# Kernel tuning notes

Hardware: AMD Instinct MI355X
Metric: run time of the kernel (lower is better)

Reference implementation:

```python
import jax, jax.numpy as jnp
import numpy as np

FS = 32000
HOP = 512
WIN_SIZES = [2048, 1024, 512, 256, 128, 64]
BAND_EDGES = [20.0, 80.0, 500.0, 1250.0, 2540.0, 4050.0, 15000.0]
ERB_STEP = 0.25
ERBS = np.arange(1.75, 39.0 + 1e-6, ERB_STEP)            # 150 ERB channels
FC = (10.0 ** (ERBS / 21.366) - 1.0) / 0.004368           # channel center freqs (Hz)
I0 = (2e-5) ** 2                                          # reference intensity (Pa^2)
LUT_X = np.linspace(0.0, 110.0, 88).astype(np.float32)    # LUT excitation grid (dB)
SIGMA = 0.08
P_INHIB = 1.5978
HALF = 8
_g = np.arange(-HALF, HALF + 1) * ERB_STEP
GAUSS = np.exp(-_g ** 2 / (2.0 * SIGMA ** 2))
GAUSS = (GAUSS / GAUSS.sum()).astype(np.float32)

def _components():
    # frequency-dependent window selection: longest window -> lowest band
    freqs, idxs = [], []
    for w, N in enumerate(WIN_SIZES):
        fb = np.arange(N // 2 + 1) * FS / N
        sel = np.where((fb >= BAND_EDGES[w]) & (fb < BAND_EDGES[w + 1]))[0]
        idxs.append(sel)
        freqs.append(fb[sel])
    return np.concatenate(freqs), idxs
COMP_FREQS, WIN_BIN_IDX = _components()  # K ~ 67 sparse components

def _roex():
    erbw = 24.673 * (0.004368 * FC + 1.0)
    p = 4.0 * FC / erbw
    g = np.abs(COMP_FREQS[:, None] / FC[None, :] - 1.0)
    return ((1.0 + p * g) * np.exp(-p * g)).astype(np.float32)
ROEX_W = _roex()  # (K, 150)

def _ear_filter(x, h):
    # Stage 1: outer/middle ear FIR, same-length output
    B, C, T = x.shape
    k = h[::-1].reshape(1, 1, -1)
    y = jax.lax.conv_general_dilated(x.reshape(B * C, 1, T), k, (1,),
                                     [(h.shape[0] // 2, h.shape[0] // 2)],
                                     dimension_numbers=("NCH", "OIH", "NCH"))
    return y.reshape(B, C, T)

def _sparse_spectrum(x):
    # Stage 2: multi-resolution FFT analysis -> linear intensities at sparse comps
    B, T = x.shape
    F = T // HOP
    pad = WIN_SIZES[0] // 2
    xp = jnp.pad(x, ((0, 0), (pad, pad)))
    centers = pad + jnp.arange(F) * HOP
    outs = []
    for N, bins in zip(WIN_SIZES, WIN_BIN_IDX):
        idx = (centers - N // 2)[:, None] + jnp.arange(N)   # (F, N)
        frames = xp[:, idx]                                 # (B, F, N)
        n = jnp.arange(N, dtype=x.dtype)
        win = 0.5 - 0.5 * jnp.cos(2.0 * jnp.pi * n / (N - 1))
        spec = jnp.fft.rfft(frames * win, axis=-1)
        amp = 2.0 * jnp.abs(spec[..., jnp.asarray(bins)]) / win.sum()
        outs.append(0.5 * amp ** 2)                          # tone intensity
    return jnp.concatenate(outs, axis=-1)                    # (B, F, K)

def _agc(x, a_att, a_rel):
    # asymmetric attack/release AGC over frame axis (axis=1)
    def step(s, xt):
        a = jnp.where(xt > s, a_att, a_rel)
        s = a * xt + (1.0 - a) * s
        return s, s
    xt = jnp.moveaxis(x, 1, 0)
    _, y = jax.lax.scan(step, jnp.zeros_like(xt[0]), xt)
    return jnp.moveaxis(y, 0, 1)

def _smooth(n):
    # Gaussian spatial smoothing along ERB-channel axis
    B, F, C = n.shape
    k = jnp.asarray(GAUSS[::-1].copy(), n.dtype).reshape(1, 1, -1)
    y = jax.lax.conv_general_dilated(n.reshape(B * F, 1, C), k, (1,),
                                     [(HALF, HALF)],
                                     dimension_numbers=("NCH", "OIH", "NCH"))
    return y.reshape(B, F, C)

def _forward(audio, ear_fir, lut_values):
    y = _ear_filter(audio, ear_fir)
    lut_x = jnp.asarray(LUT_X)
    W = jnp.asarray(ROEX_W, audio.dtype)
    stl = []
    for ch in range(2):
        I = _sparse_spectrum(y[:, ch])                       # (B, F, K)
        E = I @ W                                            # roex excitation (B, F, 150)
        E_db = 10.0 * jnp.log10(E / I0 + 1e-12)
        n_inst = jnp.interp(jnp.clip(E_db, lut_x[0], lut_x[-1]), lut_x, lut_values)
        stl.append(_agc(n_inst, 0.045, 0.033))               # short-term loudness
    sl, sr = _smooth(stl[0]), _smooth(stl[1])
    sech = lambda z: 1.0 / jnp.cosh(z)
    stl_l = (sl * sech(P_INHIB * sr)).sum(-1) / 4.0          # (B, F)
    stl_r = (sr * sech(P_INHIB * sl)).sum(-1) / 4.0
    ltl_l = _agc(stl_l[..., None], 0.01, 0.00133)[..., 0]
    ltl_r = _agc(stl_r[..., None], 0.01, 0.00133)[..., 0]
    sLoud = stl_l + stl_r
    lLoud = ltl_l + ltl_r
    mLoud = lLoud.max(axis=-1)
    return sLoud, lLoud, mLoud

def setup_inputs():
    key = jax.random.key(0)
    k1, k2, k3 = jax.random.split(key, 3)
    audio = jax.random.normal(k1, (16, 2, 320000), dtype=jnp.float32) * 0.05
    ear_fir = jax.random.normal(k2, (1025,), dtype=jnp.float32) * 0.03
    lut_values = jnp.sort(jax.random.uniform(k3, (88,), dtype=jnp.float32)) * 40.0
    return {"audio": audio, "ear_fir": ear_fir, "lut_values": lut_values}

def reference(audio, ear_fir, lut_values):
    return _forward(audio, ear_fir, lut_values)
```

## Files before the change

### kernel.cpp

```cpp
#include <hip/hip_runtime.h>
#include <hip/hip_bf16.h>
#include <math.h>

#define T_LEN   320000
#define NB      16
#define NROWS   32
#define NFRAMES 625
#define NCOMP   67
#define NCH     150
#define HOPSZ   512
#define BREP    8
#define BSZ     491520

typedef __attribute__((ext_vector_type(8))) _Float16 half8v;
typedef __attribute__((ext_vector_type(8))) short short8v;
typedef __attribute__((ext_vector_type(4))) float f32x4;

__constant__ int cW_N[6]  = {2048,1024,512,256,128,64};
__constant__ int cW_K0[6] = {2,3,8,10,11,9};
__constant__ int cW_CB[7] = {0,4,17,29,40,46,67};
__constant__ int cW_CO[7] = {0,8192,21504,27648,30464,31232,32576};
__constant__ int dNEp[6]  = {3072,2048,1536,1280,1152,1152};
__constant__ int dNEr[6]  = {3072,2048,1536,1280,1152,1088};
__constant__ int dBTb[7]  = {0,147456,245760,319488,380928,436224,491520};
__constant__ int dCPB[6]  = {12,8,6,5,5,5};
__constant__ int dCKB[7]  = {0,48,152,224,279,309,414};
__constant__ int eW[8] = {0,0,0,1,2,3,4,5};
__constant__ int eF[8] = {0,1,624,0,0,0,0,0};

__constant__ int tBb[12]   = {147456,180224,0,380928,0,436224,245760,454656,270336,473088,319488,339968};
__constant__ int tNEp[12]  = {2048,2048,3072,1152,3072,1152,1536,1152,1536,1152,1280,1280};
__constant__ int tStb[12]  = {512,512,0,960,0,992,768,992,768,992,896,896};
__constant__ int tKs0[12]  = {0,0,0,0,48,0,0,0,0,0,0,0};
__constant__ int tKs1[12]  = {64,64,48,36,96,36,48,36,48,36,40,40};
__constant__ int tJadd[12] = {4,12,0,40,0,46,17,54,25,62,29,37};
__constant__ int tNbL[12]  = {13,5,4,6,4,21,12,13,4,5,11,3};
__constant__ int tMode[12] = {0,0,1,0,2,0,0,0,0,0,0,0};
__constant__ int wStart[8] = {0,1,2,4,6,8,10,11};
__constant__ int wCnt[8]   = {1,1,2,2,2,2,1,1};

__device__ __forceinline__ unsigned short f2bf(float v) {
  unsigned u = __float_as_uint(v);
  return (unsigned short)((u + 0x7FFFu + ((u >> 16) & 1u)) >> 16);
}

__global__ __launch_bounds__(256) void setup_k(const float* __restrict__ h,
                                               const float* __restrict__ x,
                                               float2* __restrict__ coeff,
                                               float* __restrict__ Wmat,
                                               float* __restrict__ gauss,
                                               unsigned short* __restrict__ Bf,
                                               float* __restrict__ ye,
                                               unsigned short* __restrict__ Wb16) {
  __shared__ __align__(16) float sm[3585];
  const int bid = blockIdx.x, tid = threadIdx.x;
  if (bid < 167) {
    int gid = bid * 256 + tid;
    if (gid < 32576) {
      int w = 0;
      while (gid >= cW_CO[w + 1]) ++w;
      int local = gid - cW_CO[w];
      int N = cW_N[w];
      int jloc = local / N;
      int n = local - jloc * N;
      int k = cW_K0[w] + jloc;
      float win = 0.5f - 0.5f * cospif(2.0f * (float)n / (float)(N - 1));
      int r = (int)(((long long)k * (long long)n) % (long long)N);
      float ang = 2.0f * (float)r / (float)N;
      float scale = sqrtf(2.0f) / (0.5f * (float)(N - 1));
      float wc = win * scale;
      coeff[gid] = make_float2(wc * cospif(ang), wc * sinpif(ang));
    } else if (gid < 32576 + NCOMP * NCH) {
      int t = gid - 32576;
      int j = t / NCH, c = t - j * NCH;
      float erb = 1.75f + 0.25f * (float)c;
      float fc = (exp10f(erb * (1.0f / 21.366f)) - 1.0f) * (1.0f / 0.004368f);
      float erbw = 24.673f * (0.004368f * fc + 1.0f);
      float p = 4.0f * fc / erbw;
      int w = 0;
      while (j >= cW_CB[w + 1]) ++w;
      float freq = (float)(cW_K0[w] + (j - cW_CB[w])) * (32000.0f / (float)cW_N[w]);
      float g = fabsf(freq / fc - 1.0f);
      float pg = p * g;
      Wmat[j * NCH + c] = (1.0f + pg) * expf(-pg);
    } else if (gid == 32576 + NCOMP * NCH) {
      float tmp[17]; float s = 0.0f;
      for (int k = 0; k < 17; ++k) {
        float g = ((float)k - 8.0f) * 0.25f;
        tmp[k] = expf(-g * g / (2.0f * 0.08f * 0.08f));
        s += tmp[k];
      }
      for (int k = 0; k < 17; ++k) gauss[k] = tmp[k] / s;
    }
  } else if (bid < 581) {
    float* cre_l = sm;
    float* cim_l = sm + 1280;
    float* hs    = sm + 2560;
    const int b2 = bid - 167;
    int w = 0;
    while (b2 >= dCKB[w + 1]) ++w;
    const int local = b2 - dCKB[w];
    const int jloc = local / dCPB[w];
    const int chunk = local - jloc * dCPB[w];
    const int N = cW_N[w];
    const int k = cW_K0[w] + jloc;
    const int NEp = dNEp[w], NEr = dNEr[w];
    const int v0 = chunk * 256;
    const int nlo_blk = max(0, v0 - 1024);
    const int nhi_blk = min(N - 1, v0 + 255);
    const int cnt_n = nhi_blk - nlo_blk + 1;
    const float scale = sqrtf(2.0f) / (0.5f * (float)(N - 1));
    for (int i = tid; i < 1025; i += 256) hs[i] = h[i];
    for (int i = tid; i < cnt_n; i += 256) {
      int n = nlo_blk + i;
      float win = 0.5f - 0.5f * cospif(2.0f * (float)n / (float)(N - 1));
      int r = (int)(((long long)k * (long long)n) % (long long)N);
      float ang = 2.0f * (float)r / (float)N;
      float wc = win * scale;
      cre_l[i] = wc * cospif(ang);
      cim_l[i] = wc * sinpif(ang);
    }
    __syncthreads();
    const int v = v0 + tid;
    if (v >= NEp) return;
    float re = 0.0f, im = 0.0f;
    if (v < NEr) {
      const int n0 = max(nlo_blk, v - 1024);
      const int n1 = min(nhi_blk, v);
      float r0 = 0.f, r1 = 0.f, r2 = 0.f, r3 = 0.f;
      float m0 = 0.f, m1 = 0.f, m2 = 0.f, m3 = 0.f;
      int n = n0;
      const int hoff = 1024 - v, coff = -nlo_blk;
      for (; n + 3 <= n1; n += 4) {
        float h0 = hs[n + hoff],     h1 = hs[n + 1 + hoff];
        float h2 = hs[n + 2 + hoff], h3 = hs[n + 3 + hoff];
        r0 = fmaf(cre_l[n + coff],     h0, r0); m0 = fmaf(cim_l[n + coff],     h0, m0);
        r1 = fmaf(cre_l[n + 1 + coff], h1, r1); m1 = fmaf(cim_l[n + 1 + coff], h1, m1);
        r2 = fmaf(cre_l[n + 2 + coff], h2, r2); m2 = fmaf(cim_l[n + 2 + coff], h2, m2);
        r3 = fmaf(cre_l[n + 3 + coff], h3, r3); m3 = fmaf(cim_l[n + 3 + coff], h3, m3);
      }
      for (; n <= n1; ++n) {
        float hv = hs[n + hoff];
        r0 = fmaf(cre_l[n + coff], hv, r0);
        m0 = fmaf(cim_l[n + coff], hv, m0);
      }
      re = (r0 + r1) + (r2 + r3);
      im = (m0 + m1) + (m2 + m3);
    }
    size_t o0 = (size_t)dBTb[w] + (size_t)(2 * jloc) * NEp + v;
    size_t o1 = o0 + NEp;
    _Float16 hr = (_Float16)re;
    _Float16 hi2 = (_Float16)im;
    unsigned short hrb = *(unsigned short*)&hr;
    unsigned short hib = *(unsigned short*)&hi2;
#pragma unroll
    for (int cp = 0; cp < BREP; ++cp) {
      Bf[(size_t)cp * BSZ + o0] = hrb;
      Bf[(size_t)cp * BSZ + o1] = hib;
    }
  } else if (bid < 965) {
    float* xl = sm;
    float* hs = sm + 1280;
    const int b2 = bid - 581;
    const int chunk = b2 % 12, row = b2 / 12;
    const size_t rowoff = (size_t)row * T_LEN;
    const int i0 = chunk * 256;
    const int pos0 = (i0 < 1536) ? i0 : 318464 + (i0 - 1536);
    for (int i = tid; i < 1025; i += 256) hs[i] = h[i];
    for (int i = tid; i < 1280; i += 256) {
      int g = pos0 - 512 + i;
      xl[i] = ((unsigned)g < (unsigned)T_LEN) ? x[rowoff + g] : 0.0f;
    }
    __syncthreads();
    float a0 = 0.0f, a1 = 0.0f, a2 = 0.0f, a3 = 0.0f;
    const int d = tid + 1024;
    const float4* hs4 = (const float4*)hs;
    for (int m = 0; m < 1024; m += 4) {
      float4 hv = hs4[m >> 2];
      a0 = fmaf(hv.x, xl[d - m],     a0);
      a1 = fmaf(hv.y, xl[d - m - 1], a1);
      a2 = fmaf(hv.z, xl[d - m - 2], a2);
      a3 = fmaf(hv.w, xl[d - m - 3], a3);
    }
    float acc = ((a0 + a1) + (a2 + a3)) + hs[1024] * xl[d - 1024];
    ye[(size_t)row * 3072 + i0 + tid] = acc;
  } else {
    for (int u = tid; u < 160 * 96; u += 256) {
      int c = u / 96, j = u - (u / 96) * 96;
      float val = 0.0f;
      if (c < NCH && j < NCOMP) {
        float erb = 1.75f + 0.25f * (float)c;
        float fc = (exp10f(erb * (1.0f / 21.366f)) - 1.0f) * (1.0f / 0.004368f);
        float erbw = 24.673f * (0.004368f * fc + 1.0f);
        float p = 4.0f * fc / erbw;
        int w = 0;
        while (j >= cW_CB[w + 1]) ++w;
        float freq = (float)(cW_K0[w] + (j - cW_CB[w])) * (32000.0f / (float)cW_N[w]);
        float g = fabsf(freq / fc - 1.0f);
        float pg = p * g;
        val = (1.0f + pg) * expf(-pg);
      }
      Wb16[u] = f2bf(val);
    }
  }
}

#define TILE_X 18944
#define SWZ4(i) ((i) ^ ((((i) >> 9) & 15) << 3))

__global__ __launch_bounds__(512) void sparse2(const float* __restrict__ x,
                                               const unsigned short* __restrict__ Bf,
                                               const float2* __restrict__ coeff,
                                               const float* __restrict__ ye,
                                               float* __restrict__ Ibuf) {
  __shared__ __align__(16) unsigned short sxh[TILE_X];
  __shared__ float redA[512];
  const int b = blockIdx.x, tid = threadIdx.x;
  if (b < 640) {
    const int fblk = b % 20, row = b / 20;
    const int f0 = fblk * 32;
    const float* xr = x + (size_t)row * T_LEN;
    const unsigned short* Bc = Bf + (size_t)(b & (BREP - 1)) * BSZ;
    const int lo = f0 * HOPSZ - 1536;
    for (int i = 4 * tid; i < TILE_X; i += 2048) {
      const int g = lo + i;
      float v[4];
      if (g >= 0 && g + 4 <= T_LEN) {
        f32x4 p = __builtin_nontemporal_load((const f32x4*)(xr + g));
        v[0] = p[0]; v[1] = p[1]; v[2] = p[2]; v[3] = p[3];
      } else {
#pragma unroll
        for (int q = 0; q < 4; ++q) {
          int gg = g + q;
          v[q] = ((unsigned)gg < (unsigned)T_LEN) ? __builtin_nontemporal_load(xr + gg) : 0.0f;
        }
      }
      unsigned short h4[4];
#pragma unroll
      for (int q = 0; q < 4; ++q) {
        _Float16 hv = (_Float16)v[q];
        h4[q] = *(unsigned short*)&hv;
      }
      const int is = SWZ4(i);
      *(ushort4*)(sxh + is) = make_ushort4(h4[0], h4[1], h4[2], h4[3]);
    }
    __syncthreads();
    const int wv = tid >> 6, lane = tid & 63;
    const int fidx = lane & 15, kg = lane >> 4;
    const int t0 = wStart[wv], tcnt = wCnt[wv];
    f32x4 pA = (f32x4){0.f,0.f,0.f,0.f};
    f32x4 pB = (f32x4){0.f,0.f,0.f,0.f};
    for (int ti = t0; ti < t0 + tcnt; ++ti) {
      const int NEp = tNEp[ti];
      const int ks0 = tKs0[ti], ks1 = tKs1[ti];
      const unsigned short* Bp = Bc + tBb[ti] + fidx * NEp + kg * 8;
      const int ibase = fidx * 512 + tStb[ti] + kg * 8;
      f32x4 acc0 = (f32x4){0.f,0.f,0.f,0.f};
      f32x4 acc1 = (f32x4){0.f,0.f,0.f,0.f};
#pragma unroll 2
      for (int kk = ks0; kk < ks1; ++kk) {
        const int ko = kk * 32;
        half8v bv = *(const half8v*)(Bp + ko);
        half8v a0 = *(const half8v*)(sxh + SWZ4(ibase + ko));
        half8v a1 = *(const half8v*)(sxh + SWZ4(ibase + 8192 + ko));
        acc0 = __builtin_amdgcn_mfma_f32_16x16x32_f16(a0, bv, acc0, 0, 0, 0);
        acc1 = __builtin_amdgcn_mfma_f32_16x16x32_f16(a1, bv, acc1, 0, 0, 0);
      }
      const int mode = tMode[ti];
      if (mode == 0) {
        const int jadd = tJadd[ti], nbl = tNbL[ti];
        const int fh = fidx >> 1;
        const bool jvalid = !(fidx & 1) && fh < nbl;
#pragma unroll
        for (int r = 0; r < 4; ++r) {
          float v0 = acc0[r];
          float sq0 = v0 * v0;
          sq0 += __shfl_xor(sq0, 1);
          int fA = f0 + kg * 4 + r;
          if (jvalid && fA != 0)
            __builtin_nontemporal_store(sq0, &Ibuf[((size_t)row * NFRAMES + fA) * NCOMP + jadd + fh]);
          float v1 = acc1[r];
          float sq1 = v1 * v1;
          sq1 += __shfl_xor(sq1, 1);
          int fB = f0 + 16 + kg * 4 + r;
          if (jvalid && fB < NFRAMES)
            __builtin_nontemporal_store(sq1, &Ibuf[((size_t)row * NFRAMES + fB) * NCOMP + jadd + fh]);
        }
      } else if (mode == 1) {
#pragma unroll
        for (int r = 0; r < 4; ++r) {
          redA[lane * 4 + r] = acc0[r];
          redA[256 + lane * 4 + r] = acc1[r];
        }
      } else {
        pA = acc0; pB = acc1;
      }
    }
    __syncthreads();
    if (wv == 3) {
#pragma unroll
      for (int r = 0; r < 4; ++r) {
        float v0 = pA[r] + redA[lane * 4 + r];
        float sq0 = v0 * v0;
        sq0 += __shfl_xor(sq0, 1);
        int fA = f0 + kg * 4 + r;
        float v1 = pB[r] + redA[256 + lane * 4 + r];
        float sq1 = v1 * v1;
        sq1 += __shfl_xor(sq1, 1);
        int fB = f0 + 16 + kg * 4 + r;
        if (!(fidx & 1)) {
          int j = fidx >> 1;
          if (j < 4) {
            bool eA = (fA == 0) || (fA == 1) || (fA == 624);
            if (!eA) __builtin_nontemporal_store(sq0, &Ibuf[((size_t)row * NFRAMES + fA) * NCOMP + j]);
            bool eB = (fB == 1) || (fB == 624);
            if (fB < NFRAMES && !eB) __builtin_nontemporal_store(sq1, &Ibuf[((size_t)row * NFRAMES + fB) * NCOMP + j]);
          }
        }
      }
    }
  } else {
    const int row = b - 640;
    float* yl = (float*)sxh;
    for (int i = tid; i < 3072; i += 512) yl[i] = ye[(size_t)row * 3072 + i];
    __syncthreads();
    const int wv = tid >> 6, lane = tid & 63;
    const int w = eW[wv], f = eF[wv];
    const int N = cW_N[w];
    const int nb = cW_CB[w + 1] - cW_CB[w];
    for (int jl = 0; jl < nb; ++jl) {
      const float2* cf = coeff + cW_CO[w] + (size_t)jl * N;
      float re = 0.0f, im = 0.0f;
      for (int n = lane; n < N; n += 64) {
        int pos = f * HOPSZ - (N >> 1) + n;
        if ((unsigned)pos < (unsigned)T_LEN) {
          int yi = (pos < 1536) ? pos : (pos - 318464 + 1536);
          float yv = yl[yi];
          float2 cs = cf[n];
          re = fmaf(yv, cs.x, re);
          im = fmaf(yv, cs.y, im);
        }
      }
#pragma unroll
      for (int off = 32; off > 0; off >>= 1) {
        re += __shfl_xor(re, off);
        im += __shfl_xor(im, off);
      }
      if (lane == 0)
        Ibuf[((size_t)row * NFRAMES + f) * NCOMP + (cW_CB[w] + jl)] = re * re + im * im;
    }
  }
}

__global__ __launch_bounds__(256) void espec(const float* __restrict__ Ibuf,
                                             const unsigned short* __restrict__ Wb16,
                                             const float* __restrict__ lut,
                                             float* __restrict__ ninst) {
  __shared__ __align__(16) unsigned short sxA[64 * 104];
  __shared__ float luts[88];
  const int row = blockIdx.y;
  const int fB = blockIdx.x * 64;
  const int tid = threadIdx.x;
  if (tid < 88) luts[tid] = lut[tid];
  for (int u = tid; u < 64 * 52; u += 256) ((unsigned*)sxA)[u] = 0;
  __syncthreads();
  for (int u = tid; u < 64 * NCOMP; u += 256) {
    int fl = u / NCOMP, j = u - fl * NCOMP;
    int f = fB + fl;
    float v = (f < NFRAMES) ? __builtin_nontemporal_load(&Ibuf[((size_t)row * NFRAMES + f) * NCOMP + j]) : 0.0f;
    sxA[fl * 104 + j] = f2bf(v);
  }
  __syncthreads();
  const int wv = tid >> 6, lane = tid & 63;
  const int fidx = lane & 15, kg = lane >> 4;
  const unsigned short* Ap = sxA + (wv * 16 + fidx) * 104 + kg * 8;
  short8v a0 = *(const short8v*)(Ap);
  short8v a1 = *(const short8v*)(Ap + 32);
  short8v a2 = *(const short8v*)(Ap + 64);
  f32x4 acc[10];
#pragma unroll
  for (int ct = 0; ct < 10; ++ct) acc[ct] = (f32x4){0.f,0.f,0.f,0.f};
#pragma unroll
  for (int ct = 0; ct < 10; ++ct) {
    const unsigned short* Bp = Wb16 + (ct * 16 + fidx) * 96 + kg * 8;
    short8v b0 = *(const short8v*)(Bp);
    short8v b1 = *(const short8v*)(Bp + 32);
    short8v b2 = *(const short8v*)(Bp + 64);
    acc[ct] = __builtin_amdgcn_mfma_f32_16x16x32_bf16(a0, b0, acc[ct], 0, 0, 0);
    acc[ct] = __builtin_amdgcn_mfma_f32_16x16x32_bf16(a1, b1, acc[ct], 0, 0, 0);
    acc[ct] = __builtin_amdgcn_mfma_f32_16x16x32_bf16(a2, b2, acc[ct], 0, 0, 0);
  }
  const int fbase = fB + wv * 16 + kg * 4;
#pragma unroll
  for (int ct = 0; ct < 10; ++ct) {
    const int c = ct * 16 + fidx;
    if (c < NCH) {
#pragma unroll
      for (int r = 0; r < 4; ++r) {
        const int f = fbase + r;
        if (f < NFRAMES) {
          float e = acc[ct][r];
          float edb = 3.0102999566f * __log2f(fmaf(e, 2.5e9f, 1e-12f));
          float xv = fminf(fmaxf(edb, 0.0f), 110.0f);
          float u2 = xv * (87.0f / 110.0f);
          int i0 = (int)u2; if (i0 > 86) i0 = 86;
          float fr = u2 - (float)i0;
          ninst[((size_t)row * NFRAMES + f) * NCH + c] =
              fmaf(luts[i0 + 1] - luts[i0], fr, luts[i0]);
        }
      }
    }
  }
}

__global__ __launch_bounds__(64) void agc1(const float* __restrict__ ninst,
                                           float* __restrict__ stl) {
  int idx = blockIdx.x * 64 + threadIdx.x;
  if (idx >= NROWS * NCH) return;
  int row = idx / NCH, c = idx - row * NCH;
  const float* src = ninst + (size_t)row * NFRAMES * NCH + c;
  float* dst = stl + (size_t)row * NFRAMES * NCH + c;
  float buf[32], cur[32];
#pragma unroll
  for (int i = 0; i < 32; ++i) buf[i] = src[(size_t)i * NCH];
  float s = 0.0f;
  for (int fb = 0; fb < 576; fb += 32) {
#pragma unroll
    for (int i = 0; i < 32; ++i) cur[i] = buf[i];
#pragma unroll
    for (int i = 0; i < 32; ++i) buf[i] = src[(size_t)(fb + 32 + i) * NCH];
#pragma unroll
    for (int j = 0; j < 32; ++j) {
      float xv = cur[j];
      float a = (xv > s) ? 0.045f : 0.033f;
      s = a * xv + (1.0f - a) * s;
      dst[(size_t)(fb + j) * NCH] = s;
    }
  }
#pragma unroll
  for (int j = 0; j < 32; ++j) {
    float xv = buf[j];
    float a = (xv > s) ? 0.045f : 0.033f;
    s = a * xv + (1.0f - a) * s;
    dst[(size_t)(576 + j) * NCH] = s;
  }
  for (int f = 608; f < 625; ++f) {
    float xv = src[(size_t)f * NCH];
    float a = (xv > s) ? 0.045f : 0.033f;
    s = a * xv + (1.0f - a) * s;
    dst[(size_t)f * NCH] = s;
  }
}

__global__ __launch_bounds__(256) void combine(const float* __restrict__ stl,
                                               const float* __restrict__ gauss,
                                               float* __restrict__ outL,
                                               float* __restrict__ outR) {
  __shared__ float sl[8][168], sr[8][168], gsh[17];
  const int b = blockIdx.y, fb = blockIdx.x * 8;
  const int tid = threadIdx.x;
  if (tid < 17) gsh[tid] = gauss[tid];
  for (int u = tid; u < 8 * 168; u += 256) {
    int fi = u / 168, c = u - fi * 168;
    sl[fi][c] = 0.0f; sr[fi][c] = 0.0f;
  }
  __syncthreads();
  for (int u = tid; u < 8 * 300; u += 256) {
    int fi = u / 300, r = u - fi * 300;
    int f = fb + fi;
    if (f < NFRAMES) {
      int ch = (r < NCH) ? 0 : 1;
      int c = (r < NCH) ? r : r - NCH;
      float v = stl[((size_t)(b * 2 + ch) * NFRAMES + f) * NCH + c];
      if (ch == 0) sl[fi][8 + c] = v; else sr[fi][8 + c] = v;
    }
  }
  __syncthreads();
  const int wv = tid >> 6, lane = tid & 63;
#pragma unroll
  for (int fi2 = 0; fi2 < 2; ++fi2) {
    const int fi = wv * 2 + fi2;
    const int f = fb + fi;
    float pvl = 0.0f, pvr = 0.0f;
#pragma unroll
    for (int s = 0; s < 3; ++s) {
      int c = lane + 64 * s;
      if (c < NCH) {
        float smL = 0.0f, smR = 0.0f;
#pragma unroll
        for (int t = 0; t < 17; ++t) {
          smL = fmaf(gsh[t], sl[fi][c + t], smL);
          smR = fmaf(gsh[t], sr[fi][c + t], smR);
        }
        float tR = __expf(-1.5978f * smR);
        float tL = __expf(-1.5978f * smL);
        pvl += smL * (2.0f * tR / fmaf(tR, tR, 1.0f));
        pvr += smR * (2.0f * tL / fmaf(tL, tL, 1.0f));
      }
    }
#pragma unroll
    for (int off = 32; off > 0; off >>= 1) {
      pvl += __shfl_xor(pvl, off);
      pvr += __shfl_xor(pvr, off);
    }
    if (lane == 0 && f < NFRAMES) {
      outL[b * NFRAMES + f] = pvl * 0.25f;
      outR[b * NFRAMES + f] = pvr * 0.25f;
    }
  }
}

__global__ __launch_bounds__(256) void final_k(const float* __restrict__ sLst,
                                               const float* __restrict__ sRst,
                                               float* __restrict__ out) {
  __shared__ float Ls[NB][641];
  __shared__ float Rs[NB][641];
  __shared__ float Lv[NB][641];
  const int tid = threadIdx.x;
  for (int u = tid; u < NB * NFRAMES; u += 256) {
    int b = u / NFRAMES, f = u - b * NFRAMES;
    float a = sLst[u];
    float c = sRst[u];
    Ls[b][f] = a;
    Rs[b][f] = c;
    out[u] = a + c;
  }
  __syncthreads();
  if (tid < NB) {
    const int b = tid;
    float ll = 0.0f, lr = 0.0f, mx = -3.4e38f;
    for (int f = 0; f < NFRAMES; ++f) {
      float a = Ls[b][f];
      float c = Rs[b][f];
      float aa = (a > ll) ? 0.01f : 0.00133f;
      ll = aa * a + (1.0f - aa) * ll;
      float ab = (c > lr) ? 0.01f : 0.00133f;
      lr = ab * c + (1.0f - ab) * lr;
      float lv = ll + lr;
      Lv[b][f] = lv;
      mx = fmaxf(mx, lv);
    }
    out[2 * NB * NFRAMES + b] = mx;
  }
  __syncthreads();
  for (int u = tid; u < NB * NFRAMES; u += 256) {
    int b = u / NFRAMES, f = u - b * NFRAMES;
    out[NB * NFRAMES + u] = Lv[b][f];
  }
}

extern "C" void kernel_launch(void* const* d_in, const int* in_sizes, int n_in,
                              void* d_out, int out_size, void* d_ws, size_t ws_size,
                              hipStream_t stream) {
  const float* audio = (const float*)d_in[0];
  const float* ear   = (const float*)d_in[1];
  const float* lut   = (const float*)d_in[2];
  char* ws = (char*)d_ws;

  unsigned short* BfT    = (unsigned short*)(ws);
  float2*         coeffO = (float2*)(ws + 7864320);
  float*          Wmat   = (float*)(ws + 8124928);
  float*          gauss  = (float*)(ws + 8165128);
  float*          yedge  = (float*)(ws + 8165376);
  float*          Ibuf   = (float*)(ws + 8558592);
  float*          ninst  = (float*)(ws + 13918592);
  float*          stl    = (float*)(ws + 25918592);
  float*          stlL   = (float*)(ws + 37918592);
  float*          stlR   = (float*)(ws + 37958592);
  unsigned short* Wb16   = (unsigned short*)(ws + 37998592);

  hipLaunchKernelGGL(setup_k, dim3(966), dim3(256), 0, stream,
                     ear, audio, coeffO, Wmat, gauss, BfT, yedge, Wb16);
  hipLaunchKernelGGL(sparse2, dim3(672), dim3(512), 0, stream,
                     audio, BfT, coeffO, yedge, Ibuf);
  hipLaunchKernelGGL(espec, dim3(10, 32), dim3(256), 0, stream, Ibuf, Wb16, lut, ninst);
  hipLaunchKernelGGL(agc1, dim3(75), dim3(64), 0, stream, ninst, stl);
  hipLaunchKernelGGL(combine, dim3(79, 16), dim3(256), 0, stream, stl, gauss, stlL, stlR);
  hipLaunchKernelGGL(final_k, dim3(1), dim3(256), 0, stream, stlL, stlR, (float*)d_out);
}
```

Before: 188.1 us.

## Drop replicated basis copies, unused Wmat, and nontemporal load/store hints

Stops writing eight replicated copies of the fp16 FIR-folded DFT basis and has all sparse2 blocks read a single copy. It also removes computation of the unused fp32 roex matrix in setup, and replaces nontemporal loads and stores on audio and Ibuf with ordinary cached accesses. The workspace layout is compacted to match. This cuts setup write traffic and lets Ibuf stay in cache between sparse2 and espec, at the risk of more contention when many blocks read the same basis region.

Result: faster. 183.0 us, median of 2 (-2.7%).

```diff
diff --git a/kernel.cpp b/kernel.cpp
--- a/kernel.cpp
+++ b/kernel.cpp
@@ -9,8 +9,6 @@
 #define NCOMP   67
 #define NCH     150
 #define HOPSZ   512
-#define BREP    8
-#define BSZ     491520
 
 typedef __attribute__((ext_vector_type(8))) _Float16 half8v;
 typedef __attribute__((ext_vector_type(8))) short short8v;
@@ -47,7 +45,6 @@
 __global__ __launch_bounds__(256) void setup_k(const float* __restrict__ h,
                                                const float* __restrict__ x,
                                                float2* __restrict__ coeff,
-                                               float* __restrict__ Wmat,
                                                float* __restrict__ gauss,
                                                unsigned short* __restrict__ Bf,
                                                float* __restrict__ ye,
@@ -70,20 +67,7 @@
       float scale = sqrtf(2.0f) / (0.5f * (float)(N - 1));
       float wc = win * scale;
       coeff[gid] = make_float2(wc * cospif(ang), wc * sinpif(ang));
-    } else if (gid < 32576 + NCOMP * NCH) {
-      int t = gid - 32576;
-      int j = t / NCH, c = t - j * NCH;
-      float erb = 1.75f + 0.25f * (float)c;
-      float fc = (exp10f(erb * (1.0f / 21.366f)) - 1.0f) * (1.0f / 0.004368f);
-      float erbw = 24.673f * (0.004368f * fc + 1.0f);
-      float p = 4.0f * fc / erbw;
-      int w = 0;
-      while (j >= cW_CB[w + 1]) ++w;
-      float freq = (float)(cW_K0[w] + (j - cW_CB[w])) * (32000.0f / (float)cW_N[w]);
-      float g = fabsf(freq / fc - 1.0f);
-      float pg = p * g;
-      Wmat[j * NCH + c] = (1.0f + pg) * expf(-pg);
-    } else if (gid == 32576 + NCOMP * NCH) {
+    } else if (gid == 32576) {
       float tmp[17]; float s = 0.0f;
       for (int k = 0; k < 17; ++k) {
         float g = ((float)k - 8.0f) * 0.25f;
@@ -151,13 +135,8 @@
     size_t o1 = o0 + NEp;
     _Float16 hr = (_Float16)re;
     _Float16 hi2 = (_Float16)im;
-    unsigned short hrb = *(unsigned short*)&hr;
-    unsigned short hib = *(unsigned short*)&hi2;
-#pragma unroll
-    for (int cp = 0; cp < BREP; ++cp) {
-      Bf[(size_t)cp * BSZ + o0] = hrb;
-      Bf[(size_t)cp * BSZ + o1] = hib;
-    }
+    Bf[o0] = *(unsigned short*)&hr;
+    Bf[o1] = *(unsigned short*)&hi2;
   } else if (bid < 965) {
     float* xl = sm;
     float* hs = sm + 1280;
@@ -220,19 +199,18 @@
     const int fblk = b % 20, row = b / 20;
     const int f0 = fblk * 32;
     const float* xr = x + (size_t)row * T_LEN;
-    const unsigned short* Bc = Bf + (size_t)(b & (BREP - 1)) * BSZ;
     const int lo = f0 * HOPSZ - 1536;
     for (int i = 4 * tid; i < TILE_X; i += 2048) {
       const int g = lo + i;
       float v[4];
       if (g >= 0 && g + 4 <= T_LEN) {
-        f32x4 p = __builtin_nontemporal_load((const f32x4*)(xr + g));
-        v[0] = p[0]; v[1] = p[1]; v[2] = p[2]; v[3] = p[3];
+        float4 p = *(const float4*)(xr + g);
+        v[0] = p.x; v[1] = p.y; v[2] = p.z; v[3] = p.w;
       } else {
 #pragma unroll
         for (int q = 0; q < 4; ++q) {
           int gg = g + q;
-          v[q] = ((unsigned)gg < (unsigned)T_LEN) ? __builtin_nontemporal_load(xr + gg) : 0.0f;
+          v[q] = ((unsigned)gg < (unsigned)T_LEN) ? xr[gg] : 0.0f;
         }
       }
       unsigned short h4[4];
@@ -253,7 +231,7 @@
     for (int ti = t0; ti < t0 + tcnt; ++ti) {
       const int NEp = tNEp[ti];
       const int ks0 = tKs0[ti], ks1 = tKs1[ti];
-      const unsigned short* Bp = Bc + tBb[ti] + fidx * NEp + kg * 8;
+      const unsigned short* Bp = Bf + tBb[ti] + fidx * NEp + kg * 8;
       const int ibase = fidx * 512 + tStb[ti] + kg * 8;
       f32x4 acc0 = (f32x4){0.f,0.f,0.f,0.f};
       f32x4 acc1 = (f32x4){0.f,0.f,0.f,0.f};
@@ -278,13 +256,13 @@
           sq0 += __shfl_xor(sq0, 1);
           int fA = f0 + kg * 4 + r;
           if (jvalid && fA != 0)
-            __builtin_nontemporal_store(sq0, &Ibuf[((size_t)row * NFRAMES + fA) * NCOMP + jadd + fh]);
+            Ibuf[((size_t)row * NFRAMES + fA) * NCOMP + jadd + fh] = sq0;
           float v1 = acc1[r];
           float sq1 = v1 * v1;
           sq1 += __shfl_xor(sq1, 1);
           int fB = f0 + 16 + kg * 4 + r;
           if (jvalid && fB < NFRAMES)
-            __builtin_nontemporal_store(sq1, &Ibuf[((size_t)row * NFRAMES + fB) * NCOMP + jadd + fh]);
+            Ibuf[((size_t)row * NFRAMES + fB) * NCOMP + jadd + fh] = sq1;
         }
       } else if (mode == 1) {
 #pragma unroll
@@ -312,9 +290,9 @@
           int j = fidx >> 1;
           if (j < 4) {
             bool eA = (fA == 0) || (fA == 1) || (fA == 624);
-            if (!eA) __builtin_nontemporal_store(sq0, &Ibuf[((size_t)row * NFRAMES + fA) * NCOMP + j]);
+            if (!eA) Ibuf[((size_t)row * NFRAMES + fA) * NCOMP + j] = sq0;
             bool eB = (fB == 1) || (fB == 624);
-            if (fB < NFRAMES && !eB) __builtin_nontemporal_store(sq1, &Ibuf[((size_t)row * NFRAMES + fB) * NCOMP + j]);
+            if (fB < NFRAMES && !eB) Ibuf[((size_t)row * NFRAMES + fB) * NCOMP + j] = sq1;
           }
         }
       }
@@ -367,7 +345,7 @@
   for (int u = tid; u < 64 * NCOMP; u += 256) {
     int fl = u / NCOMP, j = u - fl * NCOMP;
     int f = fB + fl;
-    float v = (f < NFRAMES) ? __builtin_nontemporal_load(&Ibuf[((size_t)row * NFRAMES + f) * NCOMP + j]) : 0.0f;
+    float v = (f < NFRAMES) ? Ibuf[((size_t)row * NFRAMES + f) * NCOMP + j] : 0.0f;
     sxA[fl * 104 + j] = f2bf(v);
   }
   __syncthreads();
@@ -558,19 +536,18 @@
   char* ws = (char*)d_ws;
 
   unsigned short* BfT    = (unsigned short*)(ws);
-  float2*         coeffO = (float2*)(ws + 7864320);
-  float*          Wmat   = (float*)(ws + 8124928);
-  float*          gauss  = (float*)(ws + 8165128);
-  float*          yedge  = (float*)(ws + 8165376);
-  float*          Ibuf   = (float*)(ws + 8558592);
-  float*          ninst  = (float*)(ws + 13918592);
-  float*          stl    = (float*)(ws + 25918592);
-  float*          stlL   = (float*)(ws + 37918592);
-  float*          stlR   = (float*)(ws + 37958592);
-  unsigned short* Wb16   = (unsigned short*)(ws + 37998592);
+  float2*         coeffO = (float2*)(ws + 983040);
+  float*          gauss  = (float*)(ws + 1243648);
+  float*          yedge  = (float*)(ws + 1243904);
+  float*          Ibuf   = (float*)(ws + 1637120);
+  float*          ninst  = (float*)(ws + 6997120);
+  float*          stl    = (float*)(ws + 18997120);
+  float*          stlL   = (float*)(ws + 30997120);
+  float*          stlR   = (float*)(ws + 31037120);
+  unsigned short* Wb16   = (unsigned short*)(ws + 31077120);
 
   hipLaunchKernelGGL(setup_k, dim3(966), dim3(256), 0, stream,
-                     ear, audio, coeffO, Wmat, gauss, BfT, yedge, Wb16);
+                     ear, audio, coeffO, gauss, BfT, yedge, Wb16);
   hipLaunchKernelGGL(sparse2, dim3(672), dim3(512), 0, stream,
                      audio, BfT, coeffO, yedge, Ibuf);
   hipLaunchKernelGGL(espec, dim3(10, 32), dim3(256), 0, stream, Ibuf, Wb16, lut, ninst);
```
